# Optimization experiments

Measured on AMD Instinct MI355X. Metric: run time of the kernel, lower is better.

The kernel has to match this reference:

```python
import jax, jax.numpy as jnp
import numpy as np

UNITS = 32
BACKBONE = 64

def lecun_tanh(x):
    return 1.7159 * jnp.tanh(0.666 * x)

def setup_inputs() -> dict:
    key = jax.random.key(0)
    ks = jax.random.split(key, 6)
    B, C, T, H, W = 4, 16, 32, 64, 64
    scale_b = 1.0 / np.sqrt(C + UNITS)
    scale_h = 1.0 / np.sqrt(BACKBONE)
    return {
        "x": jax.random.normal(ks[0], (B, C, T, H, W), jnp.float32),
        "Wb": jax.random.normal(ks[1], (BACKBONE, C + UNITS), jnp.float32) * scale_b,
        "bb": jnp.zeros((BACKBONE,), jnp.float32),
        "Wff1": jax.random.normal(ks[2], (UNITS, BACKBONE), jnp.float32) * scale_h,
        "bff1": jnp.zeros((UNITS,), jnp.float32),
        "Wff2": jax.random.normal(ks[3], (UNITS, BACKBONE), jnp.float32) * scale_h,
        "bff2": jnp.zeros((UNITS,), jnp.float32),
        "Wta": jax.random.normal(ks[4], (UNITS, BACKBONE), jnp.float32) * scale_h,
        "bta": jnp.zeros((UNITS,), jnp.float32),
        "Wtb": jax.random.normal(ks[5], (UNITS, BACKBONE), jnp.float32) * scale_h,
        "btb": jnp.zeros((UNITS,), jnp.float32),
    }

def reference(x, Wb, bb, Wff1, bff1, Wff2, bff2, Wta, bta, Wtb, btb):
    # x: (B, C, T, H, W) -> time-major (T, B, C, H, W) for the scan
    xs = jnp.transpose(x, (2, 0, 1, 3, 4))
    B, C, H, W = x.shape[0], x.shape[1], x.shape[3], x.shape[4]
    h0 = jnp.zeros((B, UNITS, H, W), x.dtype)
    ts = jnp.asarray(1.0, x.dtype)  # no timespans provided -> ts = 1.0

    def head(z, Wh, bh):  # channel-wise (1x1) linear: (B,K,H,W) -> (B,U,H,W)
        return jnp.einsum('bkhw,uk->buhw', z, Wh) + bh[None, :, None, None]

    def step(h, xt):
        z = jnp.concatenate([xt, h], axis=1)  # (B, C+U, H, W)
        z = lecun_tanh(jnp.einsum('bchw,kc->bkhw', z, Wb) + bb[None, :, None, None])
        ff1 = jnp.tanh(head(z, Wff1, bff1))
        ff2 = jnp.tanh(head(z, Wff2, bff2))
        t_a = head(z, Wta, bta)
        t_b = head(z, Wtb, btb)
        t_interp = jax.nn.sigmoid(t_a * ts + t_b)
        h_new = ff1 * (1.0 - t_interp) + t_interp * ff2
        return h_new, h_new

    _, ys = jax.lax.scan(step, h0, xs)  # ys: (T, B, U, H, W)
    # stack along dim=1 (batch_first) then permute(0,2,1,3,4) -> (B, U, T, H, W)
    return jnp.transpose(ys, (1, 2, 0, 3, 4))
```

## Files before the change

kernel.cpp:

```cpp
#include <hip/hip_runtime.h>
#include <hip/hip_bf16.h>


#define CIN      16
#define UNITS    32
#define BACKBONE 64
#define CZ       48
#define TSTEPS   32
#define HW       4096
#define NPIX     16
#define NTHREADS 256
#define KPAD     64

typedef __attribute__((ext_vector_type(8))) short  short8;
typedef __attribute__((ext_vector_type(4))) short  short4v;
typedef __attribute__((ext_vector_type(8))) __bf16 bf16x8;
typedef __attribute__((ext_vector_type(4))) float  float4v;

__device__ __forceinline__ unsigned short bf16_rne(float f) {
    unsigned u = __float_as_uint(f);
    return (unsigned short)((u + 0x7FFFu + ((u >> 16) & 1u)) >> 16);
}
__device__ __forceinline__ float bf16_tof(unsigned short h) {
    return __uint_as_float(((unsigned)h) << 16);
}
__device__ __forceinline__ float tanh_fast(float x) {
    float e = __expf(2.0f * x);
    return 1.0f - __fdividef(2.0f, e + 1.0f);
}
__device__ __forceinline__ float sigmoid_fast(float x) {
    return __fdividef(1.0f, 1.0f + __expf(-x));
}
__device__ __forceinline__ float4v mfma16(bf16x8 a, bf16x8 b, float4v c) {
    return __builtin_amdgcn_mfma_f32_16x16x32_bf16(a, b, c, 0, 0, 0);
}
__device__ __forceinline__ void split8(const float* v, bf16x8& hi, bf16x8& lo) {
    short8 sh, sl;
    #pragma unroll
    for (int j = 0; j < 8; ++j) {
        unsigned short h = bf16_rne(v[j]);
        sh[j] = (short)h;
        sl[j] = (short)bf16_rne(v[j] - bf16_tof(h));
    }
    hi = __builtin_bit_cast(bf16x8, sh);
    lo = __builtin_bit_cast(bf16x8, sl);
}
__device__ __forceinline__ int swoff(int p, int k) {
    return p * KPAD + ((((k >> 3) ^ (p & 7)) << 3) | (k & 7));
}

__global__ __launch_bounds__(NTHREADS, 4)
void cfc_mfma_kernel(const float* __restrict__ x,   const float* __restrict__ Wb,
                     const float* __restrict__ bb,
                     const float* __restrict__ Wff1, const float* __restrict__ bff1,
                     const float* __restrict__ Wff2, const float* __restrict__ bff2,
                     const float* __restrict__ Wta,  const float* __restrict__ bta,
                     const float* __restrict__ Wtb,  const float* __restrict__ btb,
                     float* __restrict__ out)
{
    __shared__ unsigned short zhi[NPIX * KPAD];
    __shared__ unsigned short ahi[NPIX * KPAD];

    const int tid  = threadIdx.x;
    const int wave = tid >> 6;
    const int lane = tid & 63;
    const int ln   = lane & 15;
    const int lq   = lane >> 4;

    const int gpix = blockIdx.x * NPIX;
    const int b    = gpix >> 12;
    const int pinb = gpix & 4095;

    const int mt = wave;
    bf16x8 Abb_hi[2], Abb_lo[2];
    #pragma unroll
    for (int kt = 0; kt < 2; ++kt) {
        float v[8];
        #pragma unroll
        for (int j = 0; j < 8; ++j) {
            int k  = kt * 32 + lq * 8 + j;
            int ki = (k < CZ) ? k : (CZ - 1);
            float raw = Wb[(mt * 16 + ln) * CZ + ki];
            v[j] = (k < CZ) ? raw : 0.0f;
        }
        split8(v, Abb_hi[kt], Abb_lo[kt]);
    }
    const int hsel = ln & 3;
    const float* Whp = (hsel == 0) ? Wff1 : (hsel == 1) ? Wff2 : (hsel == 2) ? Wta : Wtb;
    bf16x8 Ah_hi[2][2], Ah_lo[2][2];
    #pragma unroll
    for (int i = 0; i < 2; ++i) {
        const int u = (wave * 2 + i) * 4 + (ln >> 2);
        #pragma unroll
        for (int kt = 0; kt < 2; ++kt) {
            float v[8];
            #pragma unroll
            for (int j = 0; j < 8; ++j) v[j] = Whp[u * BACKBONE + kt * 32 + lq * 8 + j];
            split8(v, Ah_hi[i][kt], Ah_lo[i][kt]);
        }
    }
    float bbias[4];
    #pragma unroll
    for (int r = 0; r < 4; ++r) bbias[r] = bb[mt * 16 + lq * 4 + r];
    float hbias[2][4];
    #pragma unroll
    for (int i = 0; i < 2; ++i) {
        const int u2 = (wave * 2 + i) * 4 + lq;
        hbias[i][0] = bff1[u2]; hbias[i][1] = bff2[u2];
        hbias[i][2] = bta[u2];  hbias[i][3] = btb[u2];
    }

    for (int i = tid; i < NPIX * KPAD / 2; i += NTHREADS)
        ((unsigned*)zhi)[i] = 0u;
    __syncthreads();
    const int xc = tid >> 4;
    const int xp = tid & 15;
    const float* xb = x + (size_t)(b * CIN + xc) * (TSTEPS * HW) + pinb + xp;
    const int xoff = swoff(xp, xc);
    zhi[xoff] = bf16_rne(xb[0]);

    const int zrd0 = swoff(ln, lq * 8);
    const int zrd1 = swoff(ln, 32 + lq * 8);
    const int awr  = swoff(ln, mt * 16 + lq * 4);
    const int u0   = (wave * 2 + 0) * 4 + lq;
    const int u1   = (wave * 2 + 1) * 4 + lq;
    const int ho0  = swoff(ln, CIN + u0);
    const int ho1  = swoff(ln, CIN + u1);
    float* po0 = out + (size_t)((b * UNITS + u0) * TSTEPS) * HW + pinb + ln;
    float* po1 = out + (size_t)((b * UNITS + u1) * TSTEPS) * HW + pinb + ln;
    int xoffs = HW;
    __syncthreads();

    #pragma unroll 1
    for (int t = 0; t < TSTEPS; ++t) {
        const float xv = xb[xoffs];

        {
            bf16x8 Z0 = __builtin_bit_cast(bf16x8, *(const short8*)&zhi[zrd0]);
            bf16x8 Z1 = __builtin_bit_cast(bf16x8, *(const short8*)&zhi[zrd1]);
            float4v acc = {bbias[0], bbias[1], bbias[2], bbias[3]};
            acc = mfma16(Abb_hi[0], Z0, acc);
            acc = mfma16(Abb_lo[0], Z0, acc);
            acc = mfma16(Abb_hi[1], Z1, acc);
            acc = mfma16(Abb_lo[1], Z1, acc);
            short4v ph;
            #pragma unroll
            for (int r = 0; r < 4; ++r)
                ph[r] = (short)bf16_rne(1.7159f * tanh_fast(0.666f * acc[r]));
            *(short4v*)&ahi[awr] = ph;
        }
        __syncthreads();

        {
            bf16x8 A0 = __builtin_bit_cast(bf16x8, *(const short8*)&ahi[zrd0]);
            bf16x8 A1 = __builtin_bit_cast(bf16x8, *(const short8*)&ahi[zrd1]);

            zhi[xoff] = bf16_rne(xv);

            {
                float4v acc = {hbias[0][0], hbias[0][1], hbias[0][2], hbias[0][3]};
                acc = mfma16(Ah_hi[0][0], A0, acc);
                acc = mfma16(Ah_lo[0][0], A0, acc);
                acc = mfma16(Ah_hi[0][1], A1, acc);
                acc = mfma16(Ah_lo[0][1], A1, acc);
                float f1 = tanh_fast(acc[0]);
                float f2 = tanh_fast(acc[1]);
                float ti = sigmoid_fast(acc[2] + acc[3]);
                float hn = f1 + ti * (f2 - f1);
                *po0 = hn;  po0 += HW;
                zhi[ho0] = bf16_rne(hn);
            }
            {
                float4v acc = {hbias[1][0], hbias[1][1], hbias[1][2], hbias[1][3]};
                acc = mfma16(Ah_hi[1][0], A0, acc);
                acc = mfma16(Ah_lo[1][0], A0, acc);
                acc = mfma16(Ah_hi[1][1], A1, acc);
                acc = mfma16(Ah_lo[1][1], A1, acc);
                float f1 = tanh_fast(acc[0]);
                float f2 = tanh_fast(acc[1]);
                float ti = sigmoid_fast(acc[2] + acc[3]);
                float hn = f1 + ti * (f2 - f1);
                *po1 = hn;  po1 += HW;
                zhi[ho1] = bf16_rne(hn);
            }
        }
        __syncthreads();

        xoffs += (t < TSTEPS - 2) ? HW : 0;
    }
}

extern "C" void kernel_launch(void* const* d_in, const int* in_sizes, int n_in,
                              void* d_out, int out_size, void* d_ws, size_t ws_size,
                              hipStream_t stream) {
    dim3 grid(4 * HW / NPIX);
    cfc_mfma_kernel<<<grid, NTHREADS, 0, stream>>>(
        (const float*)d_in[0], (const float*)d_in[1], (const float*)d_in[2],
        (const float*)d_in[3], (const float*)d_in[4], (const float*)d_in[5],
        (const float*)d_in[6], (const float*)d_in[7], (const float*)d_in[8],
        (const float*)d_in[9], (const float*)d_in[10],
        (float*)d_out);
}
```

Measured before the change: 171.4 us.

## Process each pixel tile with a single wave, removing block barriers

The kernel moves from four waves per 16-pixel tile to one 64-lane wave that computes all four backbone M-tiles and all eight head tiles itself. This removes both __syncthreads per timestep, since the LDS exchange now stays inside one wavefront. In exchange, each wave holds four times more weight fragments in registers and runs a serial chain of 48 MFMAs per step. Latency is now hidden only by running many single-wave blocks per CU, so register pressure and occupancy become the main risk.

```diff
diff --git a/kernel.cpp b/kernel.cpp
--- a/kernel.cpp
+++ b/kernel.cpp
@@ -9,7 +9,6 @@
 #define TSTEPS   32
 #define HW       4096
 #define NPIX     16
-#define NTHREADS 256
 #define KPAD     64
 
 typedef __attribute__((ext_vector_type(8))) short  short8;
@@ -49,8 +48,8 @@
     return p * KPAD + ((((k >> 3) ^ (p & 7)) << 3) | (k & 7));
 }
 
-__global__ __launch_bounds__(NTHREADS, 4)
-void cfc_mfma_kernel(const float* __restrict__ x,   const float* __restrict__ Wb,
+__global__ __launch_bounds__(64, 1)
+void cfc_wave_kernel(const float* __restrict__ x,   const float* __restrict__ Wb,
                      const float* __restrict__ bb,
                      const float* __restrict__ Wff1, const float* __restrict__ bff1,
                      const float* __restrict__ Wff2, const float* __restrict__ bff2,
@@ -58,12 +57,10 @@
                      const float* __restrict__ Wtb,  const float* __restrict__ btb,
                      float* __restrict__ out)
 {
-    __shared__ unsigned short zhi[NPIX * KPAD];
-    __shared__ unsigned short ahi[NPIX * KPAD];
-
-    const int tid  = threadIdx.x;
-    const int wave = tid >> 6;
-    const int lane = tid & 63;
+    __shared__ unsigned short z[NPIX * KPAD];
+    __shared__ unsigned short a[NPIX * KPAD];
+
+    const int lane = threadIdx.x;
     const int ln   = lane & 15;
     const int lq   = lane >> 4;
 
@@ -71,122 +68,123 @@
     const int b    = gpix >> 12;
     const int pinb = gpix & 4095;
 
-    const int mt = wave;
-    bf16x8 Abb_hi[2], Abb_lo[2];
-    #pragma unroll
-    for (int kt = 0; kt < 2; ++kt) {
-        float v[8];
-        #pragma unroll
-        for (int j = 0; j < 8; ++j) {
-            int k  = kt * 32 + lq * 8 + j;
-            int ki = (k < CZ) ? k : (CZ - 1);
-            float raw = Wb[(mt * 16 + ln) * CZ + ki];
-            v[j] = (k < CZ) ? raw : 0.0f;
-        }
-        split8(v, Abb_hi[kt], Abb_lo[kt]);
-    }
+    bf16x8 Wbh[4][2], Wbl[4][2];
+    #pragma unroll
+    for (int mt = 0; mt < 4; ++mt)
+        #pragma unroll
+        for (int kt = 0; kt < 2; ++kt) {
+            float v[8];
+            #pragma unroll
+            for (int j = 0; j < 8; ++j) {
+                int k  = kt * 32 + lq * 8 + j;
+                int ki = (k < CZ) ? k : (CZ - 1);
+                float raw = Wb[(mt * 16 + ln) * CZ + ki];
+                v[j] = (k < CZ) ? raw : 0.0f;
+            }
+            split8(v, Wbh[mt][kt], Wbl[mt][kt]);
+        }
     const int hsel = ln & 3;
     const float* Whp = (hsel == 0) ? Wff1 : (hsel == 1) ? Wff2 : (hsel == 2) ? Wta : Wtb;
-    bf16x8 Ah_hi[2][2], Ah_lo[2][2];
-    #pragma unroll
-    for (int i = 0; i < 2; ++i) {
-        const int u = (wave * 2 + i) * 4 + (ln >> 2);
+    bf16x8 Whh[8][2], Whl[8][2];
+    #pragma unroll
+    for (int i = 0; i < 8; ++i) {
+        const int u = i * 4 + (ln >> 2);
         #pragma unroll
         for (int kt = 0; kt < 2; ++kt) {
             float v[8];
             #pragma unroll
             for (int j = 0; j < 8; ++j) v[j] = Whp[u * BACKBONE + kt * 32 + lq * 8 + j];
-            split8(v, Ah_hi[i][kt], Ah_lo[i][kt]);
-        }
-    }
-    float bbias[4];
-    #pragma unroll
-    for (int r = 0; r < 4; ++r) bbias[r] = bb[mt * 16 + lq * 4 + r];
-    float hbias[2][4];
-    #pragma unroll
-    for (int i = 0; i < 2; ++i) {
-        const int u2 = (wave * 2 + i) * 4 + lq;
-        hbias[i][0] = bff1[u2]; hbias[i][1] = bff2[u2];
-        hbias[i][2] = bta[u2];  hbias[i][3] = btb[u2];
-    }
-
-    for (int i = tid; i < NPIX * KPAD / 2; i += NTHREADS)
-        ((unsigned*)zhi)[i] = 0u;
-    __syncthreads();
-    const int xc = tid >> 4;
-    const int xp = tid & 15;
-    const float* xb = x + (size_t)(b * CIN + xc) * (TSTEPS * HW) + pinb + xp;
-    const int xoff = swoff(xp, xc);
-    zhi[xoff] = bf16_rne(xb[0]);
+            split8(v, Whh[i][kt], Whl[i][kt]);
+        }
+    }
+    float bbias[4][4];
+    #pragma unroll
+    for (int mt = 0; mt < 4; ++mt)
+        #pragma unroll
+        for (int r = 0; r < 4; ++r) bbias[mt][r] = bb[mt * 16 + lq * 4 + r];
+    float hbias[8][4];
+    #pragma unroll
+    for (int i = 0; i < 8; ++i) {
+        const int u = i * 4 + lq;
+        hbias[i][0] = bff1[u]; hbias[i][1] = bff2[u];
+        hbias[i][2] = bta[u];  hbias[i][3] = btb[u];
+    }
+
+    #pragma unroll
+    for (int i = 0; i < (NPIX * KPAD / 2) / 64; ++i)
+        ((unsigned*)z)[lane + i * 64] = 0u;
+
+    const int cstride = TSTEPS * HW;
+    const float* xp0 = x + (size_t)(b * CIN + lq * 4) * cstride + pinb + ln;
+    const int xwr = swoff(ln, lq * 4);
+    {
+        short4v p;
+        #pragma unroll
+        for (int j = 0; j < 4; ++j) p[j] = (short)bf16_rne(xp0[j * cstride]);
+        *(short4v*)&z[xwr] = p;
+    }
 
     const int zrd0 = swoff(ln, lq * 8);
     const int zrd1 = swoff(ln, 32 + lq * 8);
-    const int awr  = swoff(ln, mt * 16 + lq * 4);
-    const int u0   = (wave * 2 + 0) * 4 + lq;
-    const int u1   = (wave * 2 + 1) * 4 + lq;
-    const int ho0  = swoff(ln, CIN + u0);
-    const int ho1  = swoff(ln, CIN + u1);
-    float* po0 = out + (size_t)((b * UNITS + u0) * TSTEPS) * HW + pinb + ln;
-    float* po1 = out + (size_t)((b * UNITS + u1) * TSTEPS) * HW + pinb + ln;
-    int xoffs = HW;
-    __syncthreads();
+    int awr[4];
+    #pragma unroll
+    for (int mt = 0; mt < 4; ++mt) awr[mt] = swoff(ln, mt * 16 + lq * 4);
+    int hwr[8];
+    #pragma unroll
+    for (int i = 0; i < 8; ++i) hwr[i] = swoff(ln, CIN + i * 4 + lq);
+    int oofs[8];
+    #pragma unroll
+    for (int i = 0; i < 8; ++i)
+        oofs[i] = ((b * UNITS + i * 4 + lq) * TSTEPS) * HW + pinb + ln;
+    int xo = HW;
 
     #pragma unroll 1
     for (int t = 0; t < TSTEPS; ++t) {
-        const float xv = xb[xoffs];
-
-        {
-            bf16x8 Z0 = __builtin_bit_cast(bf16x8, *(const short8*)&zhi[zrd0]);
-            bf16x8 Z1 = __builtin_bit_cast(bf16x8, *(const short8*)&zhi[zrd1]);
-            float4v acc = {bbias[0], bbias[1], bbias[2], bbias[3]};
-            acc = mfma16(Abb_hi[0], Z0, acc);
-            acc = mfma16(Abb_lo[0], Z0, acc);
-            acc = mfma16(Abb_hi[1], Z1, acc);
-            acc = mfma16(Abb_lo[1], Z1, acc);
+        float xv[4];
+        #pragma unroll
+        for (int j = 0; j < 4; ++j) xv[j] = xp0[j * cstride + xo];
+
+        bf16x8 Z0 = __builtin_bit_cast(bf16x8, *(const short8*)&z[zrd0]);
+        bf16x8 Z1 = __builtin_bit_cast(bf16x8, *(const short8*)&z[zrd1]);
+        #pragma unroll
+        for (int mt = 0; mt < 4; ++mt) {
+            float4v acc = {bbias[mt][0], bbias[mt][1], bbias[mt][2], bbias[mt][3]};
+            acc = mfma16(Wbh[mt][0], Z0, acc);
+            acc = mfma16(Wbl[mt][0], Z0, acc);
+            acc = mfma16(Wbh[mt][1], Z1, acc);
+            acc = mfma16(Wbl[mt][1], Z1, acc);
             short4v ph;
             #pragma unroll
             for (int r = 0; r < 4; ++r)
                 ph[r] = (short)bf16_rne(1.7159f * tanh_fast(0.666f * acc[r]));
-            *(short4v*)&ahi[awr] = ph;
-        }
-        __syncthreads();
+            *(short4v*)&a[awr[mt]] = ph;
+        }
+
+        bf16x8 A0 = __builtin_bit_cast(bf16x8, *(const short8*)&a[zrd0]);
+        bf16x8 A1 = __builtin_bit_cast(bf16x8, *(const short8*)&a[zrd1]);
+        #pragma unroll
+        for (int i = 0; i < 8; ++i) {
+            float4v acc = {hbias[i][0], hbias[i][1], hbias[i][2], hbias[i][3]};
+            acc = mfma16(Whh[i][0], A0, acc);
+            acc = mfma16(Whl[i][0], A0, acc);
+            acc = mfma16(Whh[i][1], A1, acc);
+            acc = mfma16(Whl[i][1], A1, acc);
+            float f1 = tanh_fast(acc[0]);
+            float f2 = tanh_fast(acc[1]);
+            float ti = sigmoid_fast(acc[2] + acc[3]);
+            float hn = f1 + ti * (f2 - f1);
+            out[oofs[i]] = hn;
+            oofs[i] += HW;
+            z[hwr[i]] = bf16_rne(hn);
+        }
 
         {
-            bf16x8 A0 = __builtin_bit_cast(bf16x8, *(const short8*)&ahi[zrd0]);
-            bf16x8 A1 = __builtin_bit_cast(bf16x8, *(const short8*)&ahi[zrd1]);
-
-            zhi[xoff] = bf16_rne(xv);
-
-            {
-                float4v acc = {hbias[0][0], hbias[0][1], hbias[0][2], hbias[0][3]};
-                acc = mfma16(Ah_hi[0][0], A0, acc);
-                acc = mfma16(Ah_lo[0][0], A0, acc);
-                acc = mfma16(Ah_hi[0][1], A1, acc);
-                acc = mfma16(Ah_lo[0][1], A1, acc);
-                float f1 = tanh_fast(acc[0]);
-                float f2 = tanh_fast(acc[1]);
-                float ti = sigmoid_fast(acc[2] + acc[3]);
-                float hn = f1 + ti * (f2 - f1);
-                *po0 = hn;  po0 += HW;
-                zhi[ho0] = bf16_rne(hn);
-            }
-            {
-                float4v acc = {hbias[1][0], hbias[1][1], hbias[1][2], hbias[1][3]};
-                acc = mfma16(Ah_hi[1][0], A0, acc);
-                acc = mfma16(Ah_lo[1][0], A0, acc);
-                acc = mfma16(Ah_hi[1][1], A1, acc);
-                acc = mfma16(Ah_lo[1][1], A1, acc);
-                float f1 = tanh_fast(acc[0]);
-                float f2 = tanh_fast(acc[1]);
-                float ti = sigmoid_fast(acc[2] + acc[3]);
-                float hn = f1 + ti * (f2 - f1);
-                *po1 = hn;  po1 += HW;
-                zhi[ho1] = bf16_rne(hn);
-            }
-        }
-        __syncthreads();
-
-        xoffs += (t < TSTEPS - 2) ? HW : 0;
+            short4v p;
+            #pragma unroll
+            for (int j = 0; j < 4; ++j) p[j] = (short)bf16_rne(xv[j]);
+            *(short4v*)&z[xwr] = p;
+        }
+        xo += (t < TSTEPS - 2) ? HW : 0;
     }
 }
 
@@ -194,7 +192,7 @@
                               void* d_out, int out_size, void* d_ws, size_t ws_size,
                               hipStream_t stream) {
     dim3 grid(4 * HW / NPIX);
-    cfc_mfma_kernel<<<grid, NTHREADS, 0, stream>>>(
+    cfc_wave_kernel<<<grid, 64, 0, stream>>>(
         (const float*)d_in[0], (const float*)d_in[1], (const float*)d_in[2],
         (const float*)d_in[3], (const float*)d_in[4], (const float*)d_in[5],
         (const float*)d_in[6], (const float*)d_in[7], (const float*)d_in[8],
```

Measured after the change: 174.3 us. No clear change (+1.7%).
